# Kernel tuning notes

Measured on AMD Instinct MI355X. Metric: run time of the kernel, lower is better.

Reference implementation:

```python
import jax, jax.numpy as jnp
import numpy as np

N_NODES = 50000
N_EDGES = 800000
N_GRAPHS = 1024
IN_DIM, HID, OUT_DIM = 78, 256, 128
EPS = 1e-5


def setup_inputs() -> dict:
    key = jax.random.key(0)
    ks = jax.random.split(key, 12)
    def lin(k, fi, fo):
        s = 1.0 / np.sqrt(fi)
        return jax.random.uniform(k, (fi, fo), jnp.float32, -s, s)
    inp = {
        "x_l": jax.random.normal(ks[0], (N_NODES, IN_DIM), jnp.float32),
        "edge_index_l": jax.random.randint(ks[1], (2, N_EDGES), 0, N_NODES, jnp.int64),
        "batch_l": jnp.sort(jax.random.randint(ks[2], (N_NODES,), 0, N_GRAPHS, jnp.int64)),
        # GraphConv 1: 78 -> 256 (lin_rel has bias, lin_root no bias)
        "W1_rel": lin(ks[3], IN_DIM, HID), "b1_rel": jnp.zeros((HID,), jnp.float32), "W1_root": lin(ks[4], IN_DIM, HID),
        # GraphConv 2: 256 -> 512
        "W2_rel": lin(ks[5], HID, 2 * HID), "b2_rel": jnp.zeros((2 * HID,), jnp.float32), "W2_root": lin(ks[6], HID, 2 * HID),
        # GraphConv 3: 512 -> 512
        "W3_rel": lin(ks[7], 2 * HID, 2 * HID), "b3_rel": jnp.zeros((2 * HID,), jnp.float32), "W3_root": lin(ks[8], 2 * HID, 2 * HID),
        # fc1: Linear(512 -> 128) + LayerNorm(128); Dropout(0.01) is identity in eval
        "W_fc": lin(ks[9], 2 * HID, OUT_DIM), "b_fc": jnp.zeros((OUT_DIM,), jnp.float32),
        "ln_g": jnp.ones((OUT_DIM,), jnp.float32), "ln_b": jnp.zeros((OUT_DIM,), jnp.float32),
    }
    return inp


def _graph_conv(x, src, dst, W_rel, b_rel, W_root):
    # PyG GraphConv (aggr='add'): out = lin_rel(sum_{j->i} x_j) + lin_root(x_i)
    aggr = jax.ops.segment_sum(x[src], dst, num_segments=x.shape[0])  # [N, d_in]
    return aggr @ W_rel + b_rel + x @ W_root


def reference(x_l, edge_index_l, batch_l,
              W1_rel, b1_rel, W1_root,
              W2_rel, b2_rel, W2_root,
              W3_rel, b3_rel, W3_root,
              W_fc, b_fc, ln_g, ln_b):
    src, dst = edge_index_l[0], edge_index_l[1]
    h = jax.nn.relu(_graph_conv(x_l, src, dst, W1_rel, b1_rel, W1_root))
    h = jax.nn.relu(_graph_conv(h, src, dst, W2_rel, b2_rel, W2_root))
    h = jax.nn.relu(_graph_conv(h, src, dst, W3_rel, b3_rel, W3_root))
    # fc1: Linear -> LayerNorm -> Dropout(0.01, identity in eval) -> ReLU
    z = h @ W_fc + b_fc
    mu = jnp.mean(z, axis=-1, keepdims=True)
    var = jnp.mean(jnp.square(z - mu), axis=-1, keepdims=True)
    z = (z - mu) * jax.lax.rsqrt(var + EPS) * ln_g + ln_b
    x_atom = jax.nn.relu(z)  # [N, OUT_DIM]
    pooled = jax.ops.segment_sum(x_atom, batch_l, num_segments=N_GRAPHS)  # [G, OUT_DIM]
    return (x_atom, pooled)
```

## Files before the change

kernel.cpp:

```cpp
#include <hip/hip_runtime.h>

#define N_NODES 50000
#define N_EDGES 800000
#define N_GRAPHS 1024
#define IN_DIM 78
#define K1P 96
#define HID 256
#define OUT_DIM 128

typedef unsigned short ushort_t;
typedef __attribute__((ext_vector_type(8))) short v8s;
typedef __attribute__((ext_vector_type(4))) float v4f;
typedef __attribute__((ext_vector_type(4))) unsigned int u4;
typedef __attribute__((ext_vector_type(2))) unsigned short us2;
typedef __attribute__((ext_vector_type(4))) unsigned short us4;
typedef __attribute__((ext_vector_type(8))) unsigned short us8;

__device__ __forceinline__ ushort_t f2bf(float f) {
    unsigned u = __float_as_uint(f);
    unsigned r = (u + 0x7fffu + ((u >> 16) & 1u)) >> 16;
    return (ushort_t)r;
}
__device__ __forceinline__ float bf2f(ushort_t h) {
    return __uint_as_float((unsigned)h << 16);
}

__device__ __forceinline__ void gload16(const ushort_t* g, ushort_t* l) {
    __builtin_amdgcn_global_load_lds(
        (const __attribute__((address_space(1))) void*)g,
        (__attribute__((address_space(3))) void*)l, 16, 0, 0);
}

__global__ __launch_bounds__(256)
void wt_all_kernel(const float* __restrict__ W1r, const float* __restrict__ W1o,
                   const float* __restrict__ W2r, const float* __restrict__ W2o,
                   const float* __restrict__ W3r, const float* __restrict__ W3o,
                   const float* __restrict__ Wfc, ushort_t* __restrict__ out)
{
    int i = blockIdx.x * 256 + threadIdx.x;
    if (i >= 901120) return;
    const float* W; int K, N, Kp, base;
    if      (i < 24576)  { W = W1r; K = IN_DIM; N = HID;     Kp = 96;  base = 0; }
    else if (i < 49152)  { W = W1o; K = IN_DIM; N = HID;     Kp = 96;  base = 24576; }
    else if (i < 180224) { W = W2r; K = HID;    N = 2 * HID; Kp = 256; base = 49152; }
    else if (i < 311296) { W = W2o; K = HID;    N = 2 * HID; Kp = 256; base = 180224; }
    else if (i < 573440) { W = W3r; K = 2*HID;  N = 2 * HID; Kp = 512; base = 311296; }
    else if (i < 835584) { W = W3o; K = 2*HID;  N = 2 * HID; Kp = 512; base = 573440; }
    else                 { W = Wfc; K = 2*HID;  N = OUT_DIM; Kp = 512; base = 835584; }
    int j = i - base;
    int n = j / Kp, k = j - n * Kp;
    float v = (k < K) ? W[(size_t)k * N + n] : 0.0f;
    out[i] = f2bf(v);
}

__global__ __launch_bounds__(256)
void pad_cast_kernel(const float* __restrict__ in, ushort_t* __restrict__ out,
                     int rows, int Kin, int Kout)
{
    int i = blockIdx.x * 256 + threadIdx.x;
    if (i >= rows * Kout) return;
    int r = i / Kout, k = i - r * Kout;
    out[i] = f2bf(k < Kin ? in[(size_t)r * Kin + k] : 0.0f);
}

__global__ __launch_bounds__(256)
void hist_kernel(const int* __restrict__ dstI, int* __restrict__ deg, int nE)
{
    int e = blockIdx.x * 256 + threadIdx.x;
    if (e < nE) {
        int d = dstI[e];
        if ((unsigned)d < (unsigned)N_NODES) atomicAdd(&deg[d], 1);
    }
}

__global__ __launch_bounds__(1024)
void scan1_kernel(const int* __restrict__ deg, int* __restrict__ rowptr,
                  int* __restrict__ blocksum, int n)
{
    __shared__ int s[1024];
    int b = (int)blockIdx.x, t = (int)threadIdx.x;
    int i = b * 1024 + t;
    int v = (i < n) ? deg[i] : 0;
    s[t] = v;
    __syncthreads();
    for (int off = 1; off < 1024; off <<= 1) {
        int a = (t >= off) ? s[t - off] : 0;
        __syncthreads();
        s[t] += a;
        __syncthreads();
    }
    if (i < n) rowptr[i + 1] = s[t];
    if (t == 1023) blocksum[b] = s[1023];
    if (b == 0 && t == 0) rowptr[0] = 0;
}

__global__ __launch_bounds__(64)
void scan2_kernel(int* __restrict__ blocksum, int nb)
{
    int t = (int)threadIdx.x;
    int v = (t < nb) ? blocksum[t] : 0;
    #pragma unroll
    for (int off = 1; off < 64; off <<= 1) {
        int a = __shfl_up(v, off, 64);
        if (t >= off) v += a;
    }
    if (t < nb) blocksum[t] = v;
}

__global__ __launch_bounds__(256)
void scan3_kernel(const int* __restrict__ blocksum, int* __restrict__ rowptr,
                  int* __restrict__ cursor, int n)
{
    int j = blockIdx.x * 256 + threadIdx.x;
    if (j > n) return;
    int v;
    if (j == 0) v = 0;
    else {
        int b = (j - 1) >> 10;
        v = rowptr[j] + (b >= 1 ? blocksum[b - 1] : 0);
    }
    rowptr[j] = v;
    if (j < n) cursor[j] = v;
}

__global__ __launch_bounds__(256)
void fill_kernel(const int* __restrict__ srcI, const int* __restrict__ dstI,
                 int* __restrict__ cursor, int* __restrict__ csr_src, int nE)
{
    int e = blockIdx.x * 256 + threadIdx.x;
    if (e < nE) {
        int d = dstI[e];
        int s = srcI[e];
        if ((unsigned)d < (unsigned)N_NODES && (unsigned)s < (unsigned)N_NODES) {
            int pos = atomicAdd(&cursor[d], 1);
            csr_src[pos] = s;
        }
    }
}

template<int VPT> struct VecT;
template<> struct VecT<2> { using T = us2; };
template<> struct VecT<4> { using T = us4; };
template<> struct VecT<8> { using T = us8; };

template<int VPT>
__global__ __launch_bounds__(256)
void csr_agg_wave_kernel(const ushort_t* __restrict__ feat,
                         const int* __restrict__ rowptr,
                         const int* __restrict__ csr_src,
                         ushort_t* __restrict__ out, int Ds)
{
    using T = typename VecT<VPT>::T;
    const int wv   = (int)threadIdx.x >> 6;
    const int node = (int)blockIdx.x * 4 + wv;
    if (node >= N_NODES) return;
    const int lane = (int)threadIdx.x & 63;
    const int off0 = lane * VPT;
    const bool act = off0 < Ds;
    const int off  = act ? off0 : (Ds - VPT);

    const int e0 = rowptr[node], e1 = rowptr[node + 1];
    float acc[VPT];
    #pragma unroll
    for (int i = 0; i < VPT; ++i) acc[i] = 0.0f;

    int e = e0;
    for (; e + 8 <= e1; e += 8) {
        T r[8];
        #pragma unroll
        for (int u = 0; u < 8; ++u) {
            int s = csr_src[e + u];
            r[u] = *(const T*)(feat + (size_t)s * Ds + off);
        }
        #pragma unroll
        for (int u = 0; u < 8; ++u)
            #pragma unroll
            for (int i = 0; i < VPT; ++i) acc[i] += bf2f(r[u][i]);
    }
    for (; e + 4 <= e1; e += 4) {
        T r[4];
        #pragma unroll
        for (int u = 0; u < 4; ++u) {
            int s = csr_src[e + u];
            r[u] = *(const T*)(feat + (size_t)s * Ds + off);
        }
        #pragma unroll
        for (int u = 0; u < 4; ++u)
            #pragma unroll
            for (int i = 0; i < VPT; ++i) acc[i] += bf2f(r[u][i]);
    }
    for (; e < e1; ++e) {
        int s = csr_src[e];
        T r = *(const T*)(feat + (size_t)s * Ds + off);
        #pragma unroll
        for (int i = 0; i < VPT; ++i) acc[i] += bf2f(r[i]);
    }

    if (act) {
        T o;
        #pragma unroll
        for (int i = 0; i < VPT; ++i) o[i] = f2bf(acc[i]);
        *(T*)(out + (size_t)node * Ds + off0) = o;
    }
}

__global__ __launch_bounds__(256, 3)
void mfma_gemm_kernel(const ushort_t* __restrict__ A1,
                      const ushort_t* __restrict__ A2,
                      const ushort_t* __restrict__ W1t,
                      const ushort_t* __restrict__ W2t,
                      const float* __restrict__ bias,
                      void* __restrict__ outp,
                      int M, int K, int Fo, int relu, int out_bf16)
{
    __shared__ __align__(16) ushort_t smem[17408];
    const int tid = (int)threadIdx.x;
    const int l   = tid & 63;
    const int w   = tid >> 6;
    const int q   = l >> 4;
    const int r15 = l & 15;
    const int bm  = blockIdx.y * 128;
    const int bn  = blockIdx.x * 128;
    const int wm  = w >> 1, wn = w & 1;

    const int s1 = K >> 5;
    const int nsteps = A2 ? (2 * s1) : s1;

    int aOff[2], bOff[2];
    #pragma unroll
    for (int ii = 0; ii < 2; ++ii) {
        int ar = bm + (w * 2 + ii) * 16 + r15;
        if (ar >= M) ar = M - 1;
        aOff[ii] = ar * K;
        int bc = bn + (w * 2 + ii) * 16 + r15;
        bOff[ii] = bc * K;
    }
    const int kq = q * 8;

    auto stage = [&](int step, int buf) {
        const ushort_t* A  = (step >= s1) ? A2  : A1;
        const ushort_t* Bt = (step >= s1) ? W2t : W1t;
        const int k0 = (((step >= s1) ? (step - s1) : step) << 5) + kq;
        ushort_t* db = smem + buf * 8192;
        #pragma unroll
        for (int ii = 0; ii < 2; ++ii)
            gload16(A + aOff[ii] + k0, db + (size_t)(w * 2 + ii) * 512);
        #pragma unroll
        for (int ii = 0; ii < 2; ++ii)
            gload16(Bt + bOff[ii] + k0, db + (size_t)(8 + w * 2 + ii) * 512);
    };

    v4f acc[4][4];
    #pragma unroll
    for (int mt = 0; mt < 4; ++mt)
        #pragma unroll
        for (int nt = 0; nt < 4; ++nt)
            acc[mt][nt] = (v4f){0.0f, 0.0f, 0.0f, 0.0f};

    stage(0, 0);
    for (int step = 0; step < nsteps; ++step) {
        const int cur = step & 1;
        __syncthreads();
        if (step + 1 < nsteps) stage(step + 1, cur ^ 1);
        const ushort_t* db = smem + cur * 8192;
        v8s af[4], bf[4];
        #pragma unroll
        for (int mt = 0; mt < 4; ++mt)
            af[mt] = *(const v8s*)(db + (size_t)(wm * 4 + mt) * 512 + l * 8);
        #pragma unroll
        for (int nt = 0; nt < 4; ++nt)
            bf[nt] = *(const v8s*)(db + (size_t)(8 + wn * 4 + nt) * 512 + l * 8);
        #pragma unroll
        for (int mt = 0; mt < 4; ++mt)
            #pragma unroll
            for (int nt = 0; nt < 4; ++nt)
                acc[mt][nt] = __builtin_amdgcn_mfma_f32_16x16x32_bf16(
                    af[mt], bf[nt], acc[mt][nt], 0, 0, 0);
    }

    if (out_bf16) {
        __syncthreads();
        #pragma unroll
        for (int nt = 0; nt < 4; ++nt) {
            int col = wn * 64 + nt * 16 + r15;
            float bb = bias[bn + col];
            #pragma unroll
            for (int mt = 0; mt < 4; ++mt) {
                int row0 = wm * 64 + mt * 16 + q * 4;
                #pragma unroll
                for (int p = 0; p < 4; ++p) {
                    float v = acc[mt][nt][p] + bb;
                    if (relu) v = fmaxf(v, 0.0f);
                    smem[(size_t)(row0 + p) * 136 + col] = f2bf(v);
                }
            }
        }
        __syncthreads();
        ushort_t* op = (ushort_t*)outp;
        #pragma unroll
        for (int pass = 0; pass < 8; ++pass) {
            int row = pass * 16 + (tid >> 4);
            int gr  = bm + row;
            if (gr < M) {
                u4 v = *(const u4*)(smem + (size_t)row * 136 + (tid & 15) * 8);
                *(u4*)(op + (size_t)gr * Fo + bn + (tid & 15) * 8) = v;
            }
        }
    } else {
        float* op = (float*)outp;
        #pragma unroll
        for (int nt = 0; nt < 4; ++nt) {
            int col = bn + wn * 64 + nt * 16 + r15;
            float bb = bias[col];
            #pragma unroll
            for (int mt = 0; mt < 4; ++mt) {
                #pragma unroll
                for (int p = 0; p < 4; ++p) {
                    int row = bm + wm * 64 + mt * 16 + q * 4 + p;
                    if (row < M) {
                        float v = acc[mt][nt][p] + bb;
                        if (relu) v = fmaxf(v, 0.0f);
                        op[(size_t)row * Fo + col] = v;
                    }
                }
            }
        }
    }
}

__global__ __launch_bounds__(128)
void ln_relu_pool_kernel(const float* __restrict__ z,
                         const float* __restrict__ gamma,
                         const float* __restrict__ beta,
                         const int* __restrict__ batch,
                         float* __restrict__ x_atom,
                         float* __restrict__ pooled)
{
    int row = (int)blockIdx.x;
    int t = (int)threadIdx.x;
    float v = z[(long long)row * 128 + t];

    __shared__ float red[2];
    float s = v;
    #pragma unroll
    for (int o = 32; o >= 1; o >>= 1) s += __shfl_xor(s, o, 64);
    int wave = t >> 6;
    if ((t & 63) == 0) red[wave] = s;
    __syncthreads();
    float mean = (red[0] + red[1]) * (1.0f / 128.0f);

    float d = v - mean;
    float s2 = d * d;
    #pragma unroll
    for (int o = 32; o >= 1; o >>= 1) s2 += __shfl_xor(s2, o, 64);
    __syncthreads();
    if ((t & 63) == 0) red[wave] = s2;
    __syncthreads();
    float var = (red[0] + red[1]) * (1.0f / 128.0f);

    float y = d * rsqrtf(var + 1e-5f) * gamma[t] + beta[t];
    y = fmaxf(y, 0.0f);
    x_atom[(long long)row * 128 + t] = y;
    int b = batch[row];
    if ((unsigned)b < (unsigned)N_GRAPHS)
        atomicAdd(pooled + (long long)b * 128 + t, y);
}

extern "C" void kernel_launch(void* const* d_in, const int* in_sizes, int n_in,
                              void* d_out, int out_size, void* d_ws, size_t ws_size,
                              hipStream_t stream)
{
    const float* x     = (const float*)d_in[0];
    const int*   ei    = (const int*)d_in[1];
    const int*   batch = (const int*)d_in[2];
    const float* W1r   = (const float*)d_in[3];
    const float* b1    = (const float*)d_in[4];
    const float* W1o   = (const float*)d_in[5];
    const float* W2r   = (const float*)d_in[6];
    const float* b2    = (const float*)d_in[7];
    const float* W2o   = (const float*)d_in[8];
    const float* W3r   = (const float*)d_in[9];
    const float* b3    = (const float*)d_in[10];
    const float* W3o   = (const float*)d_in[11];
    const float* Wfc   = (const float*)d_in[12];
    const float* bfc   = (const float*)d_in[13];
    const float* lng   = (const float*)d_in[14];
    const float* lnb   = (const float*)d_in[15];

    const size_t WS_NEED = 204800000;
    if (ws_size < WS_NEED) {
        hipMemsetAsync(d_out, 0, (size_t)out_size * sizeof(float), stream);
        return;
    }

    char* ws = (char*)d_ws;
    ushort_t* xb   = (ushort_t*)(ws + 0);
    ushort_t* h1   = (ushort_t*)(ws + 9600000);
    float*    z    = (float*)   (ws + 0);
    ushort_t* aggr = (ushort_t*)(ws + 35200000);
    ushort_t* h2   = (ushort_t*)(ws + 86400000);
    ushort_t* h3   = (ushort_t*)(ws + 137600000);
    int* deg    = (int*)(ws + 188800000);
    int* rowptr = (int*)(ws + 189000000);
    int* cursor = (int*)(ws + 189200128);
    int* csrsrc = (int*)(ws + 189400128);
    int* blksum = (int*)(ws + 192600128);
    ushort_t* wt = (ushort_t*)(ws + 192600512);
    ushort_t* w1r_t = wt;
    ushort_t* w1o_t = wt + 24576;
    ushort_t* w2r_t = wt + 49152;
    ushort_t* w2o_t = wt + 180224;
    ushort_t* w3r_t = wt + 311296;
    ushort_t* w3o_t = wt + 573440;
    ushort_t* wfc_t = wt + 835584;

    float* x_atom = (float*)d_out;
    float* pooled = x_atom + (size_t)N_NODES * OUT_DIM;

    const int* src = ei;
    const int* dst = ei + N_EDGES;

    wt_all_kernel<<<(901120 + 255) / 256, 256, 0, stream>>>(W1r, W1o, W2r, W2o,
                                                            W3r, W3o, Wfc, wt);
    pad_cast_kernel<<<((N_NODES * K1P) + 255) / 256, 256, 0, stream>>>(x, xb, N_NODES, IN_DIM, K1P);

    hipMemsetAsync(deg, 0, N_NODES * sizeof(int), stream);
    hist_kernel<<<(N_EDGES + 255) / 256, 256, 0, stream>>>(dst, deg, N_EDGES);
    {
        int nb = (N_NODES + 1023) / 1024;
        scan1_kernel<<<nb, 1024, 0, stream>>>(deg, rowptr, blksum, N_NODES);
        scan2_kernel<<<1, 64, 0, stream>>>(blksum, nb);
        scan3_kernel<<<(N_NODES + 1 + 255) / 256, 256, 0, stream>>>(blksum, rowptr, cursor, N_NODES);
    }
    fill_kernel<<<(N_EDGES + 255) / 256, 256, 0, stream>>>(src, dst, cursor, csrsrc, N_EDGES);

    const int GY = (N_NODES + 127) / 128;
    const int AGG_BLKS = (N_NODES + 3) / 4;

    csr_agg_wave_kernel<2><<<AGG_BLKS, 256, 0, stream>>>(xb, rowptr, csrsrc, aggr, K1P);
    {
        dim3 g(HID / 128, GY);
        mfma_gemm_kernel<<<g, 256, 0, stream>>>(aggr, xb, w1r_t, w1o_t, b1, h1,
                                                N_NODES, K1P, HID, 1, 1);
    }
    csr_agg_wave_kernel<4><<<AGG_BLKS, 256, 0, stream>>>(h1, rowptr, csrsrc, aggr, HID);
    {
        dim3 g((2 * HID) / 128, GY);
        mfma_gemm_kernel<<<g, 256, 0, stream>>>(aggr, h1, w2r_t, w2o_t, b2, h2,
                                                N_NODES, HID, 2 * HID, 1, 1);
    }
    csr_agg_wave_kernel<8><<<AGG_BLKS, 256, 0, stream>>>(h2, rowptr, csrsrc, aggr, 2 * HID);
    {
        dim3 g((2 * HID) / 128, GY);
        mfma_gemm_kernel<<<g, 256, 0, stream>>>(aggr, h2, w3r_t, w3o_t, b3, h3,
                                                N_NODES, 2 * HID, 2 * HID, 1, 1);
    }
    {
        dim3 g(OUT_DIM / 128, GY);
        mfma_gemm_kernel<<<g, 256, 0, stream>>>(h3, nullptr, wfc_t, nullptr, bfc, z,
                                                N_NODES, 2 * HID, OUT_DIM, 0, 0);
    }
    hipMemsetAsync(pooled, 0, (size_t)N_GRAPHS * OUT_DIM * sizeof(float), stream);
    ln_relu_pool_kernel<<<N_NODES, 128, 0, stream>>>(z, lng, lnb, batch, x_atom, pooled);
}
```

Before: 651.4 us.

## Fuse FC GEMM with LayerNorm, ReLU and pooling; add XCD swizzle to GEMM

Replaces the final FC GEMM plus a separate per-row LayerNorm/ReLU/pool kernel with one fused kernel. It computes the 128-wide FC tile, stages the fp32 result in LDS, then applies LayerNorm, ReLU and the pooled atomicAdd directly. This removes the fp32 z round trip through memory and one launch. The hidden-layer GEMM now uses a 1D grid with an XCD-aware block swizzle for better L2 locality, and its occupancy hint is raised from 3 to 4. The fused epilogue runs in two halves and adds LDS traffic and synchronisation.

```diff
diff --git a/kernel.cpp b/kernel.cpp
--- a/kernel.cpp
+++ b/kernel.cpp
@@ -29,6 +29,12 @@
     __builtin_amdgcn_global_load_lds(
         (const __attribute__((address_space(1))) void*)g,
         (__attribute__((address_space(3))) void*)l, 16, 0, 0);
+}
+
+__device__ __forceinline__ int xcd_swizzle(int orig, int nwg) {
+    int q = nwg >> 3, r = nwg & 7;
+    int xcd = orig & 7, i = orig >> 3;
+    return (xcd < r ? xcd * (q + 1) : r * (q + 1) + (xcd - r) * q) + i;
 }
 
 __global__ __launch_bounds__(256)
@@ -204,14 +210,14 @@
     }
 }
 
-__global__ __launch_bounds__(256, 3)
+__global__ __launch_bounds__(256, 4)
 void mfma_gemm_kernel(const ushort_t* __restrict__ A1,
                       const ushort_t* __restrict__ A2,
                       const ushort_t* __restrict__ W1t,
                       const ushort_t* __restrict__ W2t,
                       const float* __restrict__ bias,
-                      void* __restrict__ outp,
-                      int M, int K, int Fo, int relu, int out_bf16)
+                      ushort_t* __restrict__ outp,
+                      int M, int K, int Fo, int relu)
 {
     __shared__ __align__(16) ushort_t smem[17408];
     const int tid = (int)threadIdx.x;
@@ -219,9 +225,14 @@
     const int w   = tid >> 6;
     const int q   = l >> 4;
     const int r15 = l & 15;
-    const int bm  = blockIdx.y * 128;
-    const int bn  = blockIdx.x * 128;
     const int wm  = w >> 1, wn = w & 1;
+
+    const int wg = xcd_swizzle((int)blockIdx.x, (int)gridDim.x);
+    const int nx = Fo >> 7;
+    const int bx = wg % nx;
+    const int by = wg / nx;
+    const int bm = by * 128;
+    const int bn = bx * 128;
 
     const int s1 = K >> 5;
     const int nsteps = A2 ? (2 * s1) : s1;
@@ -278,92 +289,168 @@
                     af[mt], bf[nt], acc[mt][nt], 0, 0, 0);
     }
 
-    if (out_bf16) {
+    __syncthreads();
+    #pragma unroll
+    for (int nt = 0; nt < 4; ++nt) {
+        int col = wn * 64 + nt * 16 + r15;
+        float bb = bias[bn + col];
+        #pragma unroll
+        for (int mt = 0; mt < 4; ++mt) {
+            int row0 = wm * 64 + mt * 16 + q * 4;
+            #pragma unroll
+            for (int p = 0; p < 4; ++p) {
+                float v = acc[mt][nt][p] + bb;
+                if (relu) v = fmaxf(v, 0.0f);
+                smem[(size_t)(row0 + p) * 136 + col] = f2bf(v);
+            }
+        }
+    }
+    __syncthreads();
+    #pragma unroll
+    for (int pass = 0; pass < 8; ++pass) {
+        int row = pass * 16 + (tid >> 4);
+        int gr  = bm + row;
+        if (gr < M) {
+            u4 v = *(const u4*)(smem + (size_t)row * 136 + (tid & 15) * 8);
+            *(u4*)(outp + (size_t)gr * Fo + bn + (tid & 15) * 8) = v;
+        }
+    }
+}
+
+__global__ __launch_bounds__(256, 3)
+void mfma_fc_ln_kernel(const ushort_t* __restrict__ A,
+                       const ushort_t* __restrict__ Wt,
+                       const float* __restrict__ bias,
+                       const float* __restrict__ gamma,
+                       const float* __restrict__ beta,
+                       const int* __restrict__ batch,
+                       float* __restrict__ x_atom,
+                       float* __restrict__ pooled,
+                       int M, int K)
+{
+    __shared__ __align__(16) char smem_raw[34816];
+    ushort_t* smem = (ushort_t*)smem_raw;
+    float*    sf   = (float*)smem_raw;
+    const int tid = (int)threadIdx.x;
+    const int l   = tid & 63;
+    const int w   = tid >> 6;
+    const int q   = l >> 4;
+    const int r15 = l & 15;
+    const int wm  = w >> 1, wn = w & 1;
+    const int bm  = (int)blockIdx.x * 128;
+    const int nsteps = K >> 5;
+
+    int aOff[2], bOff[2];
+    #pragma unroll
+    for (int ii = 0; ii < 2; ++ii) {
+        int ar = bm + (w * 2 + ii) * 16 + r15;
+        if (ar >= M) ar = M - 1;
+        aOff[ii] = ar * K;
+        bOff[ii] = ((w * 2 + ii) * 16 + r15) * K;
+    }
+    const int kq = q * 8;
+
+    auto stage = [&](int step, int buf) {
+        const int k0 = (step << 5) + kq;
+        ushort_t* db = smem + buf * 8192;
+        #pragma unroll
+        for (int ii = 0; ii < 2; ++ii)
+            gload16(A + aOff[ii] + k0, db + (size_t)(w * 2 + ii) * 512);
+        #pragma unroll
+        for (int ii = 0; ii < 2; ++ii)
+            gload16(Wt + bOff[ii] + k0, db + (size_t)(8 + w * 2 + ii) * 512);
+    };
+
+    v4f acc[4][4];
+    #pragma unroll
+    for (int mt = 0; mt < 4; ++mt)
+        #pragma unroll
+        for (int nt = 0; nt < 4; ++nt)
+            acc[mt][nt] = (v4f){0.0f, 0.0f, 0.0f, 0.0f};
+
+    stage(0, 0);
+    for (int step = 0; step < nsteps; ++step) {
+        const int cur = step & 1;
         __syncthreads();
-        #pragma unroll
-        for (int nt = 0; nt < 4; ++nt) {
-            int col = wn * 64 + nt * 16 + r15;
-            float bb = bias[bn + col];
-            #pragma unroll
-            for (int mt = 0; mt < 4; ++mt) {
-                int row0 = wm * 64 + mt * 16 + q * 4;
+        if (step + 1 < nsteps) stage(step + 1, cur ^ 1);
+        const ushort_t* db = smem + cur * 8192;
+        v8s af[4], bf[4];
+        #pragma unroll
+        for (int mt = 0; mt < 4; ++mt)
+            af[mt] = *(const v8s*)(db + (size_t)(wm * 4 + mt) * 512 + l * 8);
+        #pragma unroll
+        for (int nt = 0; nt < 4; ++nt)
+            bf[nt] = *(const v8s*)(db + (size_t)(8 + wn * 4 + nt) * 512 + l * 8);
+        #pragma unroll
+        for (int mt = 0; mt < 4; ++mt)
+            #pragma unroll
+            for (int nt = 0; nt < 4; ++nt)
+                acc[mt][nt] = __builtin_amdgcn_mfma_f32_16x16x32_bf16(
+                    af[mt], bf[nt], acc[mt][nt], 0, 0, 0);
+    }
+
+    const int lrow = tid >> 2;
+    const int c0   = (tid & 3) * 32;
+    #pragma unroll
+    for (int half = 0; half < 2; ++half) {
+        __syncthreads();
+        if (wm == half) {
+            #pragma unroll
+            for (int nt = 0; nt < 4; ++nt) {
+                int col = wn * 64 + nt * 16 + r15;
+                float bb = bias[col];
                 #pragma unroll
-                for (int p = 0; p < 4; ++p) {
-                    float v = acc[mt][nt][p] + bb;
-                    if (relu) v = fmaxf(v, 0.0f);
-                    smem[(size_t)(row0 + p) * 136 + col] = f2bf(v);
+                for (int mt = 0; mt < 4; ++mt) {
+                    int row0 = mt * 16 + q * 4;
+                    #pragma unroll
+                    for (int p = 0; p < 4; ++p)
+                        sf[(size_t)(row0 + p) * 132 + col] = acc[mt][nt][p] + bb;
                 }
             }
         }
         __syncthreads();
-        ushort_t* op = (ushort_t*)outp;
-        #pragma unroll
-        for (int pass = 0; pass < 8; ++pass) {
-            int row = pass * 16 + (tid >> 4);
-            int gr  = bm + row;
-            if (gr < M) {
-                u4 v = *(const u4*)(smem + (size_t)row * 136 + (tid & 15) * 8);
-                *(u4*)(op + (size_t)gr * Fo + bn + (tid & 15) * 8) = v;
-            }
-        }
-    } else {
-        float* op = (float*)outp;
-        #pragma unroll
-        for (int nt = 0; nt < 4; ++nt) {
-            int col = bn + wn * 64 + nt * 16 + r15;
-            float bb = bias[col];
-            #pragma unroll
-            for (int mt = 0; mt < 4; ++mt) {
+        int gr = bm + half * 64 + lrow;
+        const float* rowp = sf + (size_t)lrow * 132 + c0;
+        float s = 0.0f;
+        #pragma unroll
+        for (int j = 0; j < 32; j += 4) {
+            v4f t = *(const v4f*)(rowp + j);
+            s += t[0] + t[1] + t[2] + t[3];
+        }
+        s += __shfl_xor(s, 1, 64);
+        s += __shfl_xor(s, 2, 64);
+        float mean = s * (1.0f / 128.0f);
+        float s2 = 0.0f;
+        #pragma unroll
+        for (int j = 0; j < 32; j += 4) {
+            v4f t = *(const v4f*)(rowp + j);
+            #pragma unroll
+            for (int k = 0; k < 4; ++k) { float d = t[k] - mean; s2 += d * d; }
+        }
+        s2 += __shfl_xor(s2, 1, 64);
+        s2 += __shfl_xor(s2, 2, 64);
+        float rstd = rsqrtf(s2 * (1.0f / 128.0f) + 1e-5f);
+        if (gr < M) {
+            int b = batch[gr];
+            bool pok = (unsigned)b < (unsigned)N_GRAPHS;
+            #pragma unroll
+            for (int j = 0; j < 32; j += 4) {
+                v4f t  = *(const v4f*)(rowp + j);
+                v4f g  = *(const v4f*)(gamma + c0 + j);
+                v4f bt = *(const v4f*)(beta + c0 + j);
+                v4f y;
                 #pragma unroll
-                for (int p = 0; p < 4; ++p) {
-                    int row = bm + wm * 64 + mt * 16 + q * 4 + p;
-                    if (row < M) {
-                        float v = acc[mt][nt][p] + bb;
-                        if (relu) v = fmaxf(v, 0.0f);
-                        op[(size_t)row * Fo + col] = v;
-                    }
+                for (int k = 0; k < 4; ++k)
+                    y[k] = fmaxf((t[k] - mean) * rstd * g[k] + bt[k], 0.0f);
+                *(v4f*)(x_atom + (size_t)gr * 128 + c0 + j) = y;
+                if (pok) {
+                    #pragma unroll
+                    for (int k = 0; k < 4; ++k)
+                        atomicAdd(pooled + (size_t)b * 128 + c0 + j + k, y[k]);
                 }
             }
         }
     }
-}
-
-__global__ __launch_bounds__(128)
-void ln_relu_pool_kernel(const float* __restrict__ z,
-                         const float* __restrict__ gamma,
-                         const float* __restrict__ beta,
-                         const int* __restrict__ batch,
-                         float* __restrict__ x_atom,
-                         float* __restrict__ pooled)
-{
-    int row = (int)blockIdx.x;
-    int t = (int)threadIdx.x;
-    float v = z[(long long)row * 128 + t];
-
-    __shared__ float red[2];
-    float s = v;
-    #pragma unroll
-    for (int o = 32; o >= 1; o >>= 1) s += __shfl_xor(s, o, 64);
-    int wave = t >> 6;
-    if ((t & 63) == 0) red[wave] = s;
-    __syncthreads();
-    float mean = (red[0] + red[1]) * (1.0f / 128.0f);
-
-    float d = v - mean;
-    float s2 = d * d;
-    #pragma unroll
-    for (int o = 32; o >= 1; o >>= 1) s2 += __shfl_xor(s2, o, 64);
-    __syncthreads();
-    if ((t & 63) == 0) red[wave] = s2;
-    __syncthreads();
-    float var = (red[0] + red[1]) * (1.0f / 128.0f);
-
-    float y = d * rsqrtf(var + 1e-5f) * gamma[t] + beta[t];
-    y = fmaxf(y, 0.0f);
-    x_atom[(long long)row * 128 + t] = y;
-    int b = batch[row];
-    if ((unsigned)b < (unsigned)N_GRAPHS)
-        atomicAdd(pooled + (long long)b * 128 + t, y);
 }
 
 extern "C" void kernel_launch(void* const* d_in, const int* in_sizes, int n_in,
@@ -396,7 +483,6 @@
     char* ws = (char*)d_ws;
     ushort_t* xb   = (ushort_t*)(ws + 0);
     ushort_t* h1   = (ushort_t*)(ws + 9600000);
-    float*    z    = (float*)   (ws + 0);
     ushort_t* aggr = (ushort_t*)(ws + 35200000);
     ushort_t* h2   = (ushort_t*)(ws + 86400000);
     ushort_t* h3   = (ushort_t*)(ws + 137600000);
@@ -438,28 +524,15 @@
     const int AGG_BLKS = (N_NODES + 3) / 4;
 
     csr_agg_wave_kernel<2><<<AGG_BLKS, 256, 0, stream>>>(xb, rowptr, csrsrc, aggr, K1P);
-    {
-        dim3 g(HID / 128, GY);
-        mfma_gemm_kernel<<<g, 256, 0, stream>>>(aggr, xb, w1r_t, w1o_t, b1, h1,
-                                                N_NODES, K1P, HID, 1, 1);
-    }
+    mfma_gemm_kernel<<<(HID / 128) * GY, 256, 0, stream>>>(aggr, xb, w1r_t, w1o_t, b1, h1,
+                                                           N_NODES, K1P, HID, 1);
     csr_agg_wave_kernel<4><<<AGG_BLKS, 256, 0, stream>>>(h1, rowptr, csrsrc, aggr, HID);
-    {
-        dim3 g((2 * HID) / 128, GY);
-        mfma_gemm_kernel<<<g, 256, 0, stream>>>(aggr, h1, w2r_t, w2o_t, b2, h2,
-                                                N_NODES, HID, 2 * HID, 1, 1);
-    }
+    mfma_gemm_kernel<<<((2 * HID) / 128) * GY, 256, 0, stream>>>(aggr, h1, w2r_t, w2o_t, b2, h2,
+                                                                 N_NODES, HID, 2 * HID, 1);
     csr_agg_wave_kernel<8><<<AGG_BLKS, 256, 0, stream>>>(h2, rowptr, csrsrc, aggr, 2 * HID);
-    {
-        dim3 g((2 * HID) / 128, GY);
-        mfma_gemm_kernel<<<g, 256, 0, stream>>>(aggr, h2, w3r_t, w3o_t, b3, h3,
-                                                N_NODES, 2 * HID, 2 * HID, 1, 1);
-    }
-    {
-        dim3 g(OUT_DIM / 128, GY);
-        mfma_gemm_kernel<<<g, 256, 0, stream>>>(h3, nullptr, wfc_t, nullptr, bfc, z,
-                                                N_NODES, 2 * HID, OUT_DIM, 0, 0);
-    }
+    mfma_gemm_kernel<<<((2 * HID) / 128) * GY, 256, 0, stream>>>(aggr, h2, w3r_t, w3o_t, b3, h3,
+                                                                 N_NODES, 2 * HID, 2 * HID, 1);
     hipMemsetAsync(pooled, 0, (size_t)N_GRAPHS * OUT_DIM * sizeof(float), stream);
-    ln_relu_pool_kernel<<<N_NODES, 128, 0, stream>>>(z, lng, lnb, batch, x_atom, pooled);
-}
+    mfma_fc_ln_kernel<<<GY, 256, 0, stream>>>(h3, wfc_t, bfc, lng, lnb, batch,
+                                              x_atom, pooled, N_NODES, 2 * HID);
+}
```

Result: slower. 1.023 ms (+57.1%).
